# Kernel optimization log

Hardware: AMD Instinct MI355X
Metric: run time of the kernel (lower is better)

The kernel has to match this reference:

```python
import jax, jax.numpy as jnp
import numpy as np

N_NODES = 50000
N_EDGES = 800000
IN_FEATS = 128
H_FEATS = 64
NUM_CLASSES = 2
K = 3
LAMBDA_MAX = 2.0  # standard upper bound for normalized-Laplacian max eigenvalue


def setup_inputs() -> dict:
    key = jax.random.key(0)
    ks = jax.random.split(key, 16)
    s = 0.05
    return {
        "in_feat": jax.random.normal(ks[0], (N_NODES, IN_FEATS), jnp.float32),
        "src": jax.random.randint(ks[1], (N_EDGES,), 0, N_NODES, jnp.int32),
        "dst": jax.random.randint(ks[2], (N_EDGES,), 0, N_NODES, jnp.int32),
        "W1": jax.random.normal(ks[3], (H_FEATS, IN_FEATS), jnp.float32) * s,
        "b1": jnp.zeros((H_FEATS,), jnp.float32),
        "W2": jax.random.normal(ks[4], (H_FEATS, H_FEATS), jnp.float32) * s,
        "b2": jnp.zeros((H_FEATS,), jnp.float32),
        "Wc1": jax.random.normal(ks[5], (H_FEATS, K * H_FEATS), jnp.float32) * s,
        "bc1": jnp.zeros((H_FEATS,), jnp.float32),
        "Wc2": jax.random.normal(ks[6], (H_FEATS, K * H_FEATS), jnp.float32) * s,
        "bc2": jnp.zeros((H_FEATS,), jnp.float32),
        "W3": jax.random.normal(ks[7], (H_FEATS, H_FEATS), jnp.float32) * s,
        "b3": jnp.zeros((H_FEATS,), jnp.float32),
        "W4": jax.random.normal(ks[8], (NUM_CLASSES, H_FEATS), jnp.float32) * s,
        "b4": jnp.zeros((NUM_CLASSES,), jnp.float32),
    }


def _cheb_conv(h, src, dst, d_invsqrt, W, b, k):
    """DGL ChebConv: Chebyshev recursion on scaled normalized Laplacian,
    concat k terms along feature dim, then Linear + relu (default activation)."""
    n = h.shape[0]
    re_norm = 2.0 / LAMBDA_MAX

    def a_norm(x):  # D^{-1/2} A D^{-1/2} x via edge-list SpMM
        msg = (x * d_invsqrt)[src]                              # [E, F]
        agg = jax.ops.segment_sum(msg, dst, num_segments=n)     # [N, F]
        return agg * d_invsqrt

    X0 = h
    Xs = [X0]
    X1 = -re_norm * a_norm(X0) + X0 * (re_norm - 1.0)
    Xs.append(X1)
    for _ in range(2, k):
        Xi = -2.0 * re_norm * a_norm(X1) + X1 * (2.0 * (re_norm - 1.0)) - X0
        Xs.append(Xi)
        X0, X1 = X1, Xi
    Xt = jnp.concatenate(Xs, axis=1)                            # [N, k*F]
    return jax.nn.relu(Xt @ W.T + b)


def reference(in_feat, src, dst, W1, b1, W2, b2, Wc1, bc1, Wc2, bc2, W3, b3, W4, b4):
    n = in_feat.shape[0]
    # in-degrees from dst, clamp(min=1), D^{-1/2}
    deg = jax.ops.segment_sum(jnp.ones_like(dst, jnp.float32), dst, num_segments=n)
    d_invsqrt = jnp.power(jnp.maximum(deg, 1.0), -0.5)[:, None]  # [N, 1]

    h = jax.nn.relu(in_feat @ W1.T + b1)
    h = jax.nn.relu(h @ W2.T + b2)
    h = _cheb_conv(h, src, dst, d_invsqrt, Wc1, bc1, K)
    h = _cheb_conv(h, src, dst, d_invsqrt, Wc2, bc2, K)
    h = jax.nn.relu(h @ W3.T + b3)
    h = h @ W4.T + b4
    return h
```

## Files before the change

### kernel.cpp

```cpp
#include <hip/hip_runtime.h>
#include <hip/hip_fp16.h>
#include <math.h>

#define NN 50000
#define NE 800000
#define INF 128
#define H 64
#define ELLCAP 64
#define NB_G ((NN + 63) / 64)
#define WOFF_W1 0
#define WOFF_W2 8192
#define WOFF_WC1 12288
#define WOFF_WC2 24576
#define WOFF_W3 36864
#define WTOT 40960
#define NB_CVTW (WTOT / 2048)

#define PSHIFT 8
#define NPART2 196
#define CAP 8192
#define NB_BINA 128
#define EPB (NE / NB_BINA)
#define EPT_A 25

typedef _Float16 half8_t __attribute__((ext_vector_type(8)));
typedef float float4_t __attribute__((ext_vector_type(4)));

__device__ __forceinline__ half8_t load_cvt8(const float* p) {
  float4 a = *(const float4*)(p);
  float4 b = *(const float4*)(p + 4);
  half8_t h;
  h[0] = (_Float16)a.x; h[1] = (_Float16)a.y; h[2] = (_Float16)a.z; h[3] = (_Float16)a.w;
  h[4] = (_Float16)b.x; h[5] = (_Float16)b.y; h[6] = (_Float16)b.z; h[7] = (_Float16)b.w;
  return h;
}

__global__ __launch_bounds__(256) void k_binA(const int* __restrict__ src, const int* __restrict__ dst,
                                              int* __restrict__ gcount, int* __restrict__ bucket,
                                              const float* __restrict__ W1, const float* __restrict__ W2,
                                              const float* __restrict__ Wc1, const float* __restrict__ Wc2,
                                              const float* __restrict__ W3, _Float16* __restrict__ w16) {
  int b = blockIdx.x;
  if (b >= NB_BINA) {
    int i0 = (b - NB_BINA) * 2048 + threadIdx.x * 8;
#pragma unroll
    for (int k = 0; k < 8; ++k) {
      int id = i0 + k;
      if (id < WTOT) {
        float v;
        if (id < WOFF_W2) v = W1[id];
        else if (id < WOFF_WC1) v = W2[id - WOFF_W2];
        else if (id < WOFF_WC2) v = Wc1[id - WOFF_WC1];
        else if (id < WOFF_W3) v = Wc2[id - WOFF_WC2];
        else v = W3[id - WOFF_W3];
        w16[id] = (_Float16)v;
      }
    }
    return;
  }
  __shared__ int s_cnt[NPART2];
  __shared__ int s_base[NPART2];
  const int tid = threadIdx.x;
  if (tid < NPART2) s_cnt[tid] = 0;
  __syncthreads();
  const int e0 = b * EPB;
  int rec[EPT_A];
  int meta[EPT_A];
#pragma unroll
  for (int i = 0; i < EPT_A; ++i) {
    int off = i * 256 + tid;
    meta[i] = -1;
    if (off < EPB) {
      int e = e0 + off;
      int d = __builtin_nontemporal_load(&dst[e]);
      int s = __builtin_nontemporal_load(&src[e]);
      int p = d >> PSHIFT;
      rec[i] = s | ((d & 255) << 16);
      int slot = atomicAdd(&s_cnt[p], 1);
      meta[i] = (p << 13) | slot;
    }
  }
  __syncthreads();
  if (tid < NPART2) s_base[tid] = atomicAdd(&gcount[tid], s_cnt[tid]);
  __syncthreads();
#pragma unroll
  for (int i = 0; i < EPT_A; ++i) {
    if (meta[i] >= 0) {
      int p = meta[i] >> 13;
      int pos = s_base[p] + (meta[i] & 8191);
      if (pos < CAP) bucket[(size_t)p * CAP + pos] = rec[i];
    }
  }
}

__global__ __launch_bounds__(256) void k_binB(const int* __restrict__ gcount, const int* __restrict__ bucket,
                                              unsigned short* __restrict__ ell, int* __restrict__ cnt,
                                              float* __restrict__ dinv32) {
  __shared__ int s_cnt[256];
  const int tid = threadIdx.x;
  const int p = blockIdx.x;
  s_cnt[tid] = 0;
  __syncthreads();
  int n = gcount[p];
  n = n < CAP ? n : CAP;
  const int* bp = bucket + (size_t)p * CAP;
  int j = tid;
  for (; j + 3 * 256 < n; j += 4 * 256) {
    int r0 = bp[j], r1 = bp[j + 256], r2 = bp[j + 512], r3 = bp[j + 768];
    int c0 = atomicAdd(&s_cnt[r0 >> 16], 1);
    int c1 = atomicAdd(&s_cnt[r1 >> 16], 1);
    int c2 = atomicAdd(&s_cnt[r2 >> 16], 1);
    int c3 = atomicAdd(&s_cnt[r3 >> 16], 1);
    if (c0 < ELLCAP) ell[((size_t)((p << PSHIFT) + (r0 >> 16)) << 6) + c0] = (unsigned short)(r0 & 0xFFFF);
    if (c1 < ELLCAP) ell[((size_t)((p << PSHIFT) + (r1 >> 16)) << 6) + c1] = (unsigned short)(r1 & 0xFFFF);
    if (c2 < ELLCAP) ell[((size_t)((p << PSHIFT) + (r2 >> 16)) << 6) + c2] = (unsigned short)(r2 & 0xFFFF);
    if (c3 < ELLCAP) ell[((size_t)((p << PSHIFT) + (r3 >> 16)) << 6) + c3] = (unsigned short)(r3 & 0xFFFF);
  }
  for (; j < n; j += 256) {
    int r = bp[j];
    int dl = r >> 16;
    int c = atomicAdd(&s_cnt[dl], 1);
    if (c < ELLCAP) ell[((size_t)((p << PSHIFT) + dl) << 6) + c] = (unsigned short)(r & 0xFFFF);
  }
  __syncthreads();
  int node = (p << PSHIFT) + tid;
  if (node < NN) {
    int c = s_cnt[tid];
    cnt[node] = c;
    dinv32[node] = 1.0f / sqrtf((float)(c < 1 ? 1 : c));
  }
}

__global__ __launch_bounds__(256) void k_mlp(const float* __restrict__ in_feat,
                                             const _Float16* __restrict__ w16,
                                             const float* __restrict__ b1,
                                             const float* __restrict__ b2,
                                             _Float16* __restrict__ X0c, int N) {
  __shared__ _Float16 Hs[64][72];
  const int tid = threadIdx.x;
  const int wave = tid >> 6;
  const int lane = tid & 63;
  const int m = lane & 15;
  const int quad = lane >> 4;
  const int rbase = blockIdx.x * 64 + wave * 16;
  int arow = rbase + m;
  arow = arow < N ? arow : N - 1;
  const float* Ap = in_feat + (size_t)arow * INF + quad * 8;
  const _Float16* B1 = w16 + WOFF_W1 + (size_t)m * INF + quad * 8;
  float4_t acc[4] = {{0.f,0.f,0.f,0.f},{0.f,0.f,0.f,0.f},{0.f,0.f,0.f,0.f},{0.f,0.f,0.f,0.f}};
#pragma unroll
  for (int k0 = 0; k0 < INF; k0 += 32) {
    half8_t a = load_cvt8(Ap + k0);
    half8_t b0 = *(const half8_t*)(B1 + k0);
    half8_t b1f = *(const half8_t*)(B1 + 16 * INF + k0);
    half8_t b2f = *(const half8_t*)(B1 + 32 * INF + k0);
    half8_t b3f = *(const half8_t*)(B1 + 48 * INF + k0);
    acc[0] = __builtin_amdgcn_mfma_f32_16x16x32_f16(a, b0, acc[0], 0, 0, 0);
    acc[1] = __builtin_amdgcn_mfma_f32_16x16x32_f16(a, b1f, acc[1], 0, 0, 0);
    acc[2] = __builtin_amdgcn_mfma_f32_16x16x32_f16(a, b2f, acc[2], 0, 0, 0);
    acc[3] = __builtin_amdgcn_mfma_f32_16x16x32_f16(a, b3f, acc[3], 0, 0, 0);
  }
#pragma unroll
  for (int i = 0; i < 4; ++i)
#pragma unroll
    for (int t = 0; t < 4; ++t)
      Hs[wave * 16 + quad * 4 + i][t * 16 + m] = (_Float16)fmaxf(acc[t][i] + b1[t * 16 + m], 0.f);
  __syncthreads();
  const _Float16* Ap2 = &Hs[wave * 16 + m][quad * 8];
  const _Float16* B2 = w16 + WOFF_W2 + (size_t)m * H + quad * 8;
  float4_t acc2[4] = {{0.f,0.f,0.f,0.f},{0.f,0.f,0.f,0.f},{0.f,0.f,0.f,0.f},{0.f,0.f,0.f,0.f}};
#pragma unroll
  for (int k0 = 0; k0 < H; k0 += 32) {
    half8_t a = *(const half8_t*)(Ap2 + k0);
    half8_t b0 = *(const half8_t*)(B2 + k0);
    half8_t b1f = *(const half8_t*)(B2 + 16 * H + k0);
    half8_t b2f = *(const half8_t*)(B2 + 32 * H + k0);
    half8_t b3f = *(const half8_t*)(B2 + 48 * H + k0);
    acc2[0] = __builtin_amdgcn_mfma_f32_16x16x32_f16(a, b0, acc2[0], 0, 0, 0);
    acc2[1] = __builtin_amdgcn_mfma_f32_16x16x32_f16(a, b1f, acc2[1], 0, 0, 0);
    acc2[2] = __builtin_amdgcn_mfma_f32_16x16x32_f16(a, b2f, acc2[2], 0, 0, 0);
    acc2[3] = __builtin_amdgcn_mfma_f32_16x16x32_f16(a, b3f, acc2[3], 0, 0, 0);
  }
#pragma unroll
  for (int i = 0; i < 4; ++i) {
    int rr = rbase + quad * 4 + i;
    if (rr < N) {
#pragma unroll
      for (int t = 0; t < 4; ++t)
        X0c[((size_t)rr << 6) + t * 16 + m] = (_Float16)fmaxf(acc2[t][i] + b2[t * 16 + m], 0.f);
    }
  }
}

__global__ __launch_bounds__(256) void k_spmm(const _Float16* __restrict__ table,
                                              const _Float16* __restrict__ auxc,
                                              _Float16* __restrict__ outc,
                                              const int* __restrict__ cnt,
                                              const float* __restrict__ dinv32,
                                              const unsigned short* __restrict__ ell,
                                              float alpha, int use_aux, int N) {
  int wv = (blockIdx.x * 256 + threadIdx.x) >> 6;
  int lane = threadIdx.x & 63;
  int node = wv * 4 + (lane >> 4);
  if (node >= N) return;
  int g = (lane >> 3) & 1;
  int c8 = (lane & 7) * 8;
  int deg0 = cnt[node];
  int deg = deg0 < ELLCAP ? deg0 : ELLCAP;
  const unsigned short* row = ell + ((size_t)node << 6);

  float acc[8] = {0.f, 0.f, 0.f, 0.f, 0.f, 0.f, 0.f, 0.f};
  int j = g;
  for (; j + 2 < deg; j += 4) {
    int s0 = row[j];
    int s1 = row[j + 2];
    float d0 = dinv32[s0];
    float d1 = dinv32[s1];
    half8_t v0 = *(const half8_t*)(table + ((size_t)s0 << 6) + c8);
    half8_t v1 = *(const half8_t*)(table + ((size_t)s1 << 6) + c8);
#pragma unroll
    for (int k = 0; k < 8; ++k) acc[k] = fmaf(d0, (float)v0[k], fmaf(d1, (float)v1[k], acc[k]));
  }
  if (j < deg) {
    int s0 = row[j];
    float d0 = dinv32[s0];
    half8_t v0 = *(const half8_t*)(table + ((size_t)s0 << 6) + c8);
#pragma unroll
    for (int k = 0; k < 8; ++k) acc[k] = fmaf(d0, (float)v0[k], acc[k]);
  }
#pragma unroll
  for (int k = 0; k < 8; ++k) acc[k] += __shfl_xor(acc[k], 8);
  if (g == 0) {
    float a = alpha * dinv32[node];
    float r[8];
#pragma unroll
    for (int k = 0; k < 8; ++k) r[k] = a * acc[k];
    if (use_aux) {
      half8_t x = *(const half8_t*)(auxc + ((size_t)node << 6) + c8);
#pragma unroll
      for (int k = 0; k < 8; ++k) r[k] -= (float)x[k];
    }
    half8_t ro;
#pragma unroll
    for (int k = 0; k < 8; ++k) ro[k] = (_Float16)r[k];
    *(half8_t*)(outc + ((size_t)node << 6) + c8) = ro;
  }
}

__global__ __launch_bounds__(256) void k_gemm192(const _Float16* __restrict__ A0,
                                                 const _Float16* __restrict__ A1,
                                                 const _Float16* __restrict__ A2,
                                                 const _Float16* __restrict__ B,
                                                 const float* __restrict__ bias,
                                                 _Float16* __restrict__ outc, int N) {
  const int tid = threadIdx.x;
  const int wave = tid >> 6;
  const int lane = tid & 63;
  const int m = lane & 15;
  const int quad = lane >> 4;
  const int rbase = blockIdx.x * 64 + wave * 16;
  int arow = rbase + m;
  arow = arow < N ? arow : N - 1;
  const size_t ro = ((size_t)arow << 6) + quad * 8;
  const _Float16* Bp = B + (size_t)m * 192 + quad * 8;
  float4_t acc[4] = {{0.f,0.f,0.f,0.f},{0.f,0.f,0.f,0.f},{0.f,0.f,0.f,0.f},{0.f,0.f,0.f,0.f}};
#pragma unroll
  for (int k0 = 0; k0 < 192; k0 += 32) {
    half8_t a;
    if (k0 < 64) a = *(const half8_t*)(A0 + ro + k0);
    else if (k0 < 128) a = *(const half8_t*)(A1 + ro + (k0 - 64));
    else a = *(const half8_t*)(A2 + ro + (k0 - 128));
    half8_t b0 = *(const half8_t*)(Bp + k0);
    half8_t b1f = *(const half8_t*)(Bp + 16 * 192 + k0);
    half8_t b2f = *(const half8_t*)(Bp + 32 * 192 + k0);
    half8_t b3f = *(const half8_t*)(Bp + 48 * 192 + k0);
    acc[0] = __builtin_amdgcn_mfma_f32_16x16x32_f16(a, b0, acc[0], 0, 0, 0);
    acc[1] = __builtin_amdgcn_mfma_f32_16x16x32_f16(a, b1f, acc[1], 0, 0, 0);
    acc[2] = __builtin_amdgcn_mfma_f32_16x16x32_f16(a, b2f, acc[2], 0, 0, 0);
    acc[3] = __builtin_amdgcn_mfma_f32_16x16x32_f16(a, b3f, acc[3], 0, 0, 0);
  }
#pragma unroll
  for (int i = 0; i < 4; ++i) {
    int rr = rbase + quad * 4 + i;
    if (rr < N) {
#pragma unroll
      for (int t = 0; t < 4; ++t)
        outc[((size_t)rr << 6) + t * 16 + m] = (_Float16)fmaxf(acc[t][i] + bias[t * 16 + m], 0.f);
    }
  }
}

__global__ __launch_bounds__(256) void k_tail(const _Float16* __restrict__ A0,
                                              const _Float16* __restrict__ A1,
                                              const _Float16* __restrict__ A2,
                                              const _Float16* __restrict__ w16,
                                              const float* __restrict__ bc2,
                                              const float* __restrict__ b3,
                                              const float* __restrict__ W4,
                                              const float* __restrict__ b4,
                                              float* __restrict__ out, int N) {
  __shared__ _Float16 Hs2[64][72];
  __shared__ float Hs3[64][65];
  const int tid = threadIdx.x;
  const int wave = tid >> 6;
  const int lane = tid & 63;
  const int m = lane & 15;
  const int quad = lane >> 4;
  const int rbase = blockIdx.x * 64 + wave * 16;
  int arow = rbase + m;
  arow = arow < N ? arow : N - 1;
  {
    const size_t ro = ((size_t)arow << 6) + quad * 8;
    const _Float16* Bp = w16 + WOFF_WC2 + (size_t)m * 192 + quad * 8;
    float4_t acc[4] = {{0.f,0.f,0.f,0.f},{0.f,0.f,0.f,0.f},{0.f,0.f,0.f,0.f},{0.f,0.f,0.f,0.f}};
#pragma unroll
    for (int k0 = 0; k0 < 192; k0 += 32) {
      half8_t a;
      if (k0 < 64) a = *(const half8_t*)(A0 + ro + k0);
      else if (k0 < 128) a = *(const half8_t*)(A1 + ro + (k0 - 64));
      else a = *(const half8_t*)(A2 + ro + (k0 - 128));
      half8_t b0 = *(const half8_t*)(Bp + k0);
      half8_t b1f = *(const half8_t*)(Bp + 16 * 192 + k0);
      half8_t b2f = *(const half8_t*)(Bp + 32 * 192 + k0);
      half8_t b3f = *(const half8_t*)(Bp + 48 * 192 + k0);
      acc[0] = __builtin_amdgcn_mfma_f32_16x16x32_f16(a, b0, acc[0], 0, 0, 0);
      acc[1] = __builtin_amdgcn_mfma_f32_16x16x32_f16(a, b1f, acc[1], 0, 0, 0);
      acc[2] = __builtin_amdgcn_mfma_f32_16x16x32_f16(a, b2f, acc[2], 0, 0, 0);
      acc[3] = __builtin_amdgcn_mfma_f32_16x16x32_f16(a, b3f, acc[3], 0, 0, 0);
    }
#pragma unroll
    for (int i = 0; i < 4; ++i)
#pragma unroll
      for (int t = 0; t < 4; ++t)
        Hs2[wave * 16 + quad * 4 + i][t * 16 + m] =
            (_Float16)fmaxf(acc[t][i] + bc2[t * 16 + m], 0.f);
  }
  __syncthreads();
  {
    const _Float16* Ap = &Hs2[wave * 16 + m][quad * 8];
    const _Float16* Bp = w16 + WOFF_W3 + (size_t)m * H + quad * 8;
    float4_t acc[4] = {{0.f,0.f,0.f,0.f},{0.f,0.f,0.f,0.f},{0.f,0.f,0.f,0.f},{0.f,0.f,0.f,0.f}};
#pragma unroll
    for (int k0 = 0; k0 < H; k0 += 32) {
      half8_t a = *(const half8_t*)(Ap + k0);
      half8_t b0 = *(const half8_t*)(Bp + k0);
      half8_t b1f = *(const half8_t*)(Bp + 16 * H + k0);
      half8_t b2f = *(const half8_t*)(Bp + 32 * H + k0);
      half8_t b3f = *(const half8_t*)(Bp + 48 * H + k0);
      acc[0] = __builtin_amdgcn_mfma_f32_16x16x32_f16(a, b0, acc[0], 0, 0, 0);
      acc[1] = __builtin_amdgcn_mfma_f32_16x16x32_f16(a, b1f, acc[1], 0, 0, 0);
      acc[2] = __builtin_amdgcn_mfma_f32_16x16x32_f16(a, b2f, acc[2], 0, 0, 0);
      acc[3] = __builtin_amdgcn_mfma_f32_16x16x32_f16(a, b3f, acc[3], 0, 0, 0);
    }
#pragma unroll
    for (int i = 0; i < 4; ++i)
#pragma unroll
      for (int t = 0; t < 4; ++t)
        Hs3[wave * 16 + quad * 4 + i][t * 16 + m] = fmaxf(acc[t][i] + b3[t * 16 + m], 0.f);
  }
  __syncthreads();
  if (tid < 128) {
    int r = tid >> 1;
    int c = tid & 1;
    int row = blockIdx.x * 64 + r;
    if (row < N) {
      const float* w4 = W4 + c * 64;
      float s = 0.f;
#pragma unroll
      for (int k = 0; k < 64; ++k) s = fmaf(Hs3[r][k], w4[k], s);
      out[(size_t)row * 2 + c] = s + b4[c];
    }
  }
}

extern "C" void kernel_launch(void* const* d_in, const int* in_sizes, int n_in,
                              void* d_out, int out_size, void* d_ws, size_t ws_size,
                              hipStream_t stream) {
  const float* in_feat = (const float*)d_in[0];
  const int* src = (const int*)d_in[1];
  const int* dst = (const int*)d_in[2];
  const float* W1 = (const float*)d_in[3];
  const float* b1 = (const float*)d_in[4];
  const float* W2 = (const float*)d_in[5];
  const float* b2 = (const float*)d_in[6];
  const float* Wc1 = (const float*)d_in[7];
  const float* bc1 = (const float*)d_in[8];
  const float* Wc2 = (const float*)d_in[9];
  const float* bc2 = (const float*)d_in[10];
  const float* W3 = (const float*)d_in[11];
  const float* b3 = (const float*)d_in[12];
  const float* W4 = (const float*)d_in[13];
  const float* b4 = (const float*)d_in[14];
  float* out = (float*)d_out;

  char* ws = (char*)d_ws;
  size_t o = 0;
  auto carve = [&](size_t bytes) -> void* {
    o = (o + 255) & ~(size_t)255;
    void* p = ws + o;
    o += bytes;
    return p;
  };
  int* cnt = (int*)carve((size_t)NN * 4);
  unsigned short* ell = (unsigned short*)carve((size_t)NN * ELLCAP * 2);
  float* dinv32 = (float*)carve((size_t)NN * 4);
  _Float16* w16 = (_Float16*)carve((size_t)WTOT * 2);
  _Float16* X0c = (_Float16*)carve((size_t)NN * H * 2);
  _Float16* X1c = (_Float16*)carve((size_t)NN * H * 2);
  _Float16* X2c = (_Float16*)carve((size_t)NN * H * 2);
  _Float16* Y0c = (_Float16*)carve((size_t)NN * H * 2);
  _Float16* Y1c = (_Float16*)carve((size_t)NN * H * 2);
  _Float16* Y2c = (_Float16*)carve((size_t)NN * H * 2);
  int* gcount = (int*)carve((size_t)NPART2 * 4);
  int* bucket = (int*)Y0c;
  (void)ws_size; (void)in_sizes; (void)n_in; (void)out_size;

  const int NB_W4 = (NN + 15) / 16;

  hipMemsetAsync(gcount, 0, (size_t)NPART2 * 4, stream);
  k_binA<<<NB_BINA + NB_CVTW, 256, 0, stream>>>(src, dst, gcount, bucket, W1, W2, Wc1, Wc2, W3, w16);
  k_binB<<<NPART2, 256, 0, stream>>>(gcount, bucket, ell, cnt, dinv32);
  k_mlp<<<NB_G, 256, 0, stream>>>(in_feat, w16, b1, b2, X0c, NN);
  k_spmm<<<NB_W4, 256, 0, stream>>>(X0c, (const _Float16*)nullptr, X1c, cnt, dinv32, ell, -1.f, 0, NN);
  k_spmm<<<NB_W4, 256, 0, stream>>>(X1c, X0c, X2c, cnt, dinv32, ell, -2.f, 1, NN);
  k_gemm192<<<NB_G, 256, 0, stream>>>(X0c, X1c, X2c, w16 + WOFF_WC1, bc1, Y0c, NN);
  k_spmm<<<NB_W4, 256, 0, stream>>>(Y0c, (const _Float16*)nullptr, Y1c, cnt, dinv32, ell, -1.f, 0, NN);
  k_spmm<<<NB_W4, 256, 0, stream>>>(Y1c, Y0c, Y2c, cnt, dinv32, ell, -2.f, 1, NN);
  k_tail<<<NB_G, 256, 0, stream>>>(Y0c, Y1c, Y2c, w16, bc2, b3, W4, b4, out, NN);
}
```

Before: 242.8 us.

## Pre-scale gather tables by D^-1/2 and widen SpMM to 8 lanes per node

```diff
diff --git a/kernel.cpp b/kernel.cpp
--- a/kernel.cpp
+++ b/kernel.cpp
@@ -135,7 +135,9 @@
                                              const _Float16* __restrict__ w16,
                                              const float* __restrict__ b1,
                                              const float* __restrict__ b2,
-                                             _Float16* __restrict__ X0c, int N) {
+                                             const float* __restrict__ dinv32,
+                                             _Float16* __restrict__ X0c,
+                                             _Float16* __restrict__ X0s, int N) {
   __shared__ _Float16 Hs[64][72];
   const int tid = threadIdx.x;
   const int wave = tid >> 6;
@@ -185,65 +187,87 @@
   for (int i = 0; i < 4; ++i) {
     int rr = rbase + quad * 4 + i;
     if (rr < N) {
-#pragma unroll
-      for (int t = 0; t < 4; ++t)
-        X0c[((size_t)rr << 6) + t * 16 + m] = (_Float16)fmaxf(acc2[t][i] + b2[t * 16 + m], 0.f);
-    }
-  }
-}
-
-__global__ __launch_bounds__(256) void k_spmm(const _Float16* __restrict__ table,
+      float dn = dinv32[rr];
+#pragma unroll
+      for (int t = 0; t < 4; ++t) {
+        float v = fmaxf(acc2[t][i] + b2[t * 16 + m], 0.f);
+        X0c[((size_t)rr << 6) + t * 16 + m] = (_Float16)v;
+        X0s[((size_t)rr << 6) + t * 16 + m] = (_Float16)(dn * v);
+      }
+    }
+  }
+}
+
+__global__ __launch_bounds__(256) void k_spmm(const _Float16* __restrict__ tabs,
                                               const _Float16* __restrict__ auxc,
                                               _Float16* __restrict__ outc,
+                                              _Float16* __restrict__ outs,
                                               const int* __restrict__ cnt,
                                               const float* __restrict__ dinv32,
                                               const unsigned short* __restrict__ ell,
                                               float alpha, int use_aux, int N) {
   int wv = (blockIdx.x * 256 + threadIdx.x) >> 6;
   int lane = threadIdx.x & 63;
-  int node = wv * 4 + (lane >> 4);
+  int node = wv * 8 + (lane >> 3);
   if (node >= N) return;
-  int g = (lane >> 3) & 1;
   int c8 = (lane & 7) * 8;
   int deg0 = cnt[node];
   int deg = deg0 < ELLCAP ? deg0 : ELLCAP;
   const unsigned short* row = ell + ((size_t)node << 6);
 
   float acc[8] = {0.f, 0.f, 0.f, 0.f, 0.f, 0.f, 0.f, 0.f};
-  int j = g;
-  for (; j + 2 < deg; j += 4) {
-    int s0 = row[j];
-    int s1 = row[j + 2];
-    float d0 = dinv32[s0];
-    float d1 = dinv32[s1];
-    half8_t v0 = *(const half8_t*)(table + ((size_t)s0 << 6) + c8);
-    half8_t v1 = *(const half8_t*)(table + ((size_t)s1 << 6) + c8);
-#pragma unroll
-    for (int k = 0; k < 8; ++k) acc[k] = fmaf(d0, (float)v0[k], fmaf(d1, (float)v1[k], acc[k]));
-  }
-  if (j < deg) {
-    int s0 = row[j];
-    float d0 = dinv32[s0];
-    half8_t v0 = *(const half8_t*)(table + ((size_t)s0 << 6) + c8);
-#pragma unroll
-    for (int k = 0; k < 8; ++k) acc[k] = fmaf(d0, (float)v0[k], acc[k]);
-  }
-#pragma unroll
-  for (int k = 0; k < 8; ++k) acc[k] += __shfl_xor(acc[k], 8);
-  if (g == 0) {
-    float a = alpha * dinv32[node];
-    float r[8];
-#pragma unroll
-    for (int k = 0; k < 8; ++k) r[k] = a * acc[k];
-    if (use_aux) {
-      half8_t x = *(const half8_t*)(auxc + ((size_t)node << 6) + c8);
-#pragma unroll
-      for (int k = 0; k < 8; ++k) r[k] -= (float)x[k];
-    }
-    half8_t ro;
-#pragma unroll
-    for (int k = 0; k < 8; ++k) ro[k] = (_Float16)r[k];
-    *(half8_t*)(outc + ((size_t)node << 6) + c8) = ro;
+  int j = 0;
+  for (; j + 7 < deg; j += 8) {
+    ushort4 ra = *(const ushort4*)(row + j);
+    ushort4 rb = *(const ushort4*)(row + j + 4);
+    half8_t v0 = *(const half8_t*)(tabs + (((unsigned)ra.x) << 6) + c8);
+    half8_t v1 = *(const half8_t*)(tabs + (((unsigned)ra.y) << 6) + c8);
+    half8_t v2 = *(const half8_t*)(tabs + (((unsigned)ra.z) << 6) + c8);
+    half8_t v3 = *(const half8_t*)(tabs + (((unsigned)ra.w) << 6) + c8);
+    half8_t v4 = *(const half8_t*)(tabs + (((unsigned)rb.x) << 6) + c8);
+    half8_t v5 = *(const half8_t*)(tabs + (((unsigned)rb.y) << 6) + c8);
+    half8_t v6 = *(const half8_t*)(tabs + (((unsigned)rb.z) << 6) + c8);
+    half8_t v7 = *(const half8_t*)(tabs + (((unsigned)rb.w) << 6) + c8);
+#pragma unroll
+    for (int k = 0; k < 8; ++k)
+      acc[k] += (((float)v0[k] + (float)v1[k]) + ((float)v2[k] + (float)v3[k])) +
+                (((float)v4[k] + (float)v5[k]) + ((float)v6[k] + (float)v7[k]));
+  }
+  for (; j + 3 < deg; j += 4) {
+    ushort4 ra = *(const ushort4*)(row + j);
+    half8_t v0 = *(const half8_t*)(tabs + (((unsigned)ra.x) << 6) + c8);
+    half8_t v1 = *(const half8_t*)(tabs + (((unsigned)ra.y) << 6) + c8);
+    half8_t v2 = *(const half8_t*)(tabs + (((unsigned)ra.z) << 6) + c8);
+    half8_t v3 = *(const half8_t*)(tabs + (((unsigned)ra.w) << 6) + c8);
+#pragma unroll
+    for (int k = 0; k < 8; ++k)
+      acc[k] += (((float)v0[k] + (float)v1[k]) + ((float)v2[k] + (float)v3[k]));
+  }
+  for (; j < deg; ++j) {
+    unsigned s = row[j];
+    half8_t v0 = *(const half8_t*)(tabs + (s << 6) + c8);
+#pragma unroll
+    for (int k = 0; k < 8; ++k) acc[k] += (float)v0[k];
+  }
+  float dn = dinv32[node];
+  float a = alpha * dn;
+  float r[8];
+#pragma unroll
+  for (int k = 0; k < 8; ++k) r[k] = a * acc[k];
+  if (use_aux) {
+    half8_t x = *(const half8_t*)(auxc + ((size_t)node << 6) + c8);
+#pragma unroll
+    for (int k = 0; k < 8; ++k) r[k] -= (float)x[k];
+  }
+  half8_t ro;
+#pragma unroll
+  for (int k = 0; k < 8; ++k) ro[k] = (_Float16)r[k];
+  *(half8_t*)(outc + ((size_t)node << 6) + c8) = ro;
+  if (outs) {
+    half8_t rs;
+#pragma unroll
+    for (int k = 0; k < 8; ++k) rs[k] = (_Float16)(dn * r[k]);
+    *(half8_t*)(outs + ((size_t)node << 6) + c8) = rs;
   }
 }
 
@@ -252,7 +276,9 @@
                                                  const _Float16* __restrict__ A2,
                                                  const _Float16* __restrict__ B,
                                                  const float* __restrict__ bias,
-                                                 _Float16* __restrict__ outc, int N) {
+                                                 const float* __restrict__ dinv32,
+                                                 _Float16* __restrict__ outc,
+                                                 _Float16* __restrict__ outs, int N) {
   const int tid = threadIdx.x;
   const int wave = tid >> 6;
   const int lane = tid & 63;
@@ -283,9 +309,13 @@
   for (int i = 0; i < 4; ++i) {
     int rr = rbase + quad * 4 + i;
     if (rr < N) {
-#pragma unroll
-      for (int t = 0; t < 4; ++t)
-        outc[((size_t)rr << 6) + t * 16 + m] = (_Float16)fmaxf(acc[t][i] + bias[t * 16 + m], 0.f);
+      float dn = dinv32[rr];
+#pragma unroll
+      for (int t = 0; t < 4; ++t) {
+        float v = fmaxf(acc[t][i] + bias[t * 16 + m], 0.f);
+        outc[((size_t)rr << 6) + t * 16 + m] = (_Float16)v;
+        outs[((size_t)rr << 6) + t * 16 + m] = (_Float16)(dn * v);
+      }
     }
   }
 }
@@ -406,25 +436,29 @@
   float* dinv32 = (float*)carve((size_t)NN * 4);
   _Float16* w16 = (_Float16*)carve((size_t)WTOT * 2);
   _Float16* X0c = (_Float16*)carve((size_t)NN * H * 2);
+  _Float16* X0s = (_Float16*)carve((size_t)NN * H * 2);
   _Float16* X1c = (_Float16*)carve((size_t)NN * H * 2);
+  _Float16* X1s = (_Float16*)carve((size_t)NN * H * 2);
   _Float16* X2c = (_Float16*)carve((size_t)NN * H * 2);
   _Float16* Y0c = (_Float16*)carve((size_t)NN * H * 2);
+  _Float16* Y0s = (_Float16*)carve((size_t)NN * H * 2);
   _Float16* Y1c = (_Float16*)carve((size_t)NN * H * 2);
+  _Float16* Y1s = (_Float16*)carve((size_t)NN * H * 2);
   _Float16* Y2c = (_Float16*)carve((size_t)NN * H * 2);
   int* gcount = (int*)carve((size_t)NPART2 * 4);
   int* bucket = (int*)Y0c;
   (void)ws_size; (void)in_sizes; (void)n_in; (void)out_size;
 
-  const int NB_W4 = (NN + 15) / 16;
+  const int NB_S = (NN + 31) / 32;
 
   hipMemsetAsync(gcount, 0, (size_t)NPART2 * 4, stream);
   k_binA<<<NB_BINA + NB_CVTW, 256, 0, stream>>>(src, dst, gcount, bucket, W1, W2, Wc1, Wc2, W3, w16);
   k_binB<<<NPART2, 256, 0, stream>>>(gcount, bucket, ell, cnt, dinv32);
-  k_mlp<<<NB_G, 256, 0, stream>>>(in_feat, w16, b1, b2, X0c, NN);
-  k_spmm<<<NB_W4, 256, 0, stream>>>(X0c, (const _Float16*)nullptr, X1c, cnt, dinv32, ell, -1.f, 0, NN);
-  k_spmm<<<NB_W4, 256, 0, stream>>>(X1c, X0c, X2c, cnt, dinv32, ell, -2.f, 1, NN);
-  k_gemm192<<<NB_G, 256, 0, stream>>>(X0c, X1c, X2c, w16 + WOFF_WC1, bc1, Y0c, NN);
-  k_spmm<<<NB_W4, 256, 0, stream>>>(Y0c, (const _Float16*)nullptr, Y1c, cnt, dinv32, ell, -1.f, 0, NN);
-  k_spmm<<<NB_W4, 256, 0, stream>>>(Y1c, Y0c, Y2c, cnt, dinv32, ell, -2.f, 1, NN);
+  k_mlp<<<NB_G, 256, 0, stream>>>(in_feat, w16, b1, b2, dinv32, X0c, X0s, NN);
+  k_spmm<<<NB_S, 256, 0, stream>>>(X0s, (const _Float16*)nullptr, X1c, X1s, cnt, dinv32, ell, -1.f, 0, NN);
+  k_spmm<<<NB_S, 256, 0, stream>>>(X1s, X0c, X2c, (_Float16*)nullptr, cnt, dinv32, ell, -2.f, 1, NN);
+  k_gemm192<<<NB_G, 256, 0, stream>>>(X0c, X1c, X2c, w16 + WOFF_WC1, bc1, dinv32, Y0c, Y0s, NN);
+  k_spmm<<<NB_S, 256, 0, stream>>>(Y0s, (const _Float16*)nullptr, Y1c, Y1s, cnt, dinv32, ell, -1.f, 0, NN);
+  k_spmm<<<NB_S, 256, 0, stream>>>(Y1s, Y0c, Y2c, (_Float16*)nullptr, cnt, dinv32, ell, -2.f, 1, NN);
   k_tail<<<NB_G, 256, 0, stream>>>(Y0c, Y1c, Y2c, w16, bc2, b3, W4, b4, out, NN);
 }
```

Result: slower. 251.1 us (+3.4%).
